# Performance work log

Measured on AMD Instinct MI355X. Metric: run time of the kernel, lower is better.

Reference implementation:

```python
import jax, jax.numpy as jnp
import numpy as np
from jax import lax

B, DIM, H, W = 8, 256, 48, 48
HEADS, DH = 8, 32
K, S = 5, 2
P = K // 2
SCALE = DH ** -0.5
EPS = 1e-5


def setup_inputs() -> dict:
    key = jax.random.key(0)
    ks = jax.random.split(key, 12)
    w = lambda k, sh: jax.random.normal(k, sh, jnp.float32) * 0.02
    return {
        'x': jax.random.normal(ks[0], (B, DIM, H, W), jnp.float32),
        'kv': jax.random.normal(ks[1], (B, DIM, H, W), jnp.float32),
        'wq': w(ks[2], (DIM, DIM)), 'bq': jnp.zeros((DIM,), jnp.float32),
        'wk': w(ks[3], (DIM, DIM)), 'bk': jnp.zeros((DIM,), jnp.float32),
        'wv': w(ks[4], (DIM, DIM)), 'bv': jnp.zeros((DIM,), jnp.float32),
        'w_dw': w(ks[5], (DH, 1, K, K)), 'b_dw': jnp.zeros((DH,), jnp.float32),
        'ln_w': jnp.ones((DH,), jnp.float32), 'ln_b': jnp.zeros((DH,), jnp.float32),
        'w_off': w(ks[6], (2, DH)),
        'wo': w(ks[7], (DIM, DIM)), 'bo': jnp.zeros((DIM,), jnp.float32),
    }


def conv1x1(x, w, b=None):
    # x: (B, Cin, H, W), w: (Cout, Cin)
    y = jnp.einsum('oc,bchw->bohw', w, x)
    return y if b is None else y + b[None, :, None, None]


def grid_sample_bilinear(inp, grid):
    # inp: (N, C, Hh, Ww); grid: (N, Hg, Wg, 2) in (x, y), align_corners=True
    N, C, Hh, Ww = inp.shape
    gx = (grid[..., 0] + 1.0) * 0.5 * (Ww - 1)
    gy = (grid[..., 1] + 1.0) * 0.5 * (Hh - 1)
    x0 = jnp.floor(gx)
    y0 = jnp.floor(gy)
    wx = gx - x0  # frac weights for x1/y1 corners
    wy = gy - y0
    x0i = jnp.clip(x0.astype(jnp.int32), 0, Ww - 1)
    x1i = jnp.clip(x0.astype(jnp.int32) + 1, 0, Ww - 1)
    y0i = jnp.clip(y0.astype(jnp.int32), 0, Hh - 1)
    y1i = jnp.clip(y0.astype(jnp.int32) + 1, 0, Hh - 1)
    flat = inp.reshape(N, C, Hh * Ww)
    n = grid.shape[1] * grid.shape[2]

    def gather(yi, xi):
        idx = (yi * Ww + xi).reshape(N, 1, n)
        return jnp.take_along_axis(flat, jnp.broadcast_to(idx, (N, C, n)), axis=2)

    w00 = ((1 - wx) * (1 - wy)).reshape(N, 1, n)
    w01 = (wx * (1 - wy)).reshape(N, 1, n)
    w10 = ((1 - wx) * wy).reshape(N, 1, n)
    w11 = (wx * wy).reshape(N, 1, n)
    return (w00 * gather(y0i, x0i) + w01 * gather(y0i, x1i)
            + w10 * gather(y1i, x0i) + w11 * gather(y1i, x1i))  # (N, C, n)


def reference(x, kv, wq, bq, wk, bk, wv, bv, w_dw, b_dw, ln_w, ln_b, w_off, wo, bo):
    q = conv1x1(x, wq, bq)                      # (B, DIM, H, W)
    q_off = q.reshape(B * HEADS, DH, H, W)      # per-head channels
    # depthwise offset conv
    t = lax.conv_general_dilated(q_off, w_dw, (S, S), [(P, P), (P, P)],
                                 feature_group_count=DH,
                                 dimension_numbers=('NCHW', 'OIHW', 'NCHW'))
    t = t + b_dw[None, :, None, None]
    Hk, Wk = t.shape[2], t.shape[3]
    n = Hk * Wk
    # LayerNormProxy: LN over channel dim
    t = t.transpose(0, 2, 3, 1)                 # (BH, Hk, Wk, DH)
    mu = t.mean(-1, keepdims=True)
    var = ((t - mu) ** 2).mean(-1, keepdims=True)
    t = (t - mu) / jnp.sqrt(var + EPS) * ln_w + ln_b
    t = jax.nn.gelu(t, approximate=False)
    offset = jnp.einsum('oc,bhwc->bhwo', w_off, t)  # (BH, Hk, Wk, 2) as (y, x)
    # reference points, normalized to [-1, 1]
    ref_y = (jnp.linspace(0.5, Hk - 0.5, Hk, dtype=jnp.float32) / (Hk - 1.0)) * 2.0 - 1.0
    ref_x = (jnp.linspace(0.5, Wk - 0.5, Wk, dtype=jnp.float32) / (Wk - 1.0)) * 2.0 - 1.0
    ref = jnp.stack(jnp.meshgrid(ref_y, ref_x, indexing='ij'), axis=-1)  # (Hk, Wk, 2)
    pos = jnp.clip(offset + ref[None], -1.0, 1.0)
    grid = pos[..., ::-1]                       # (x, y) order for sampling
    kvs = grid_sample_bilinear(kv.reshape(B * HEADS, DH, H, W), grid)  # (BH, DH, n)
    kv4 = kvs.reshape(B, DIM, 1, n)
    k = conv1x1(kv4, wk, bk).reshape(B * HEADS, DH, n)
    v = conv1x1(kv4, wv, bv).reshape(B * HEADS, DH, n)
    qf = q.reshape(B * HEADS, DH, H * W)
    attn = jax.nn.softmax(jnp.einsum('bcm,bcn->bmn', qf, k) * SCALE, axis=2)
    out = jnp.einsum('bmn,bcn->bcm', attn, v).reshape(B, DIM, H, W)
    return conv1x1(out, wo, bo)
```

## Files before the change

### kernel.cpp

```cpp
#include <hip/hip_runtime.h>
#include <hip/hip_bf16.h>
#include <cstddef>

#define BB 8
#define DIM 256
#define HH 48
#define WW 48
#define HW 2304
#define HEADS 8
#define DH 32
#define BH 64
#define HK 24
#define WK 24
#define NN 576
#define SCALE 0.17677669529663687f
#define EPSF 1e-5f

typedef __attribute__((ext_vector_type(8))) short short8;
typedef __attribute__((ext_vector_type(4))) float f32x4;

static __device__ inline short f2bf_s(float f) {
  __hip_bfloat16 h = __float2bfloat16(f);
  return *reinterpret_cast<short*>(&h);
}

static __device__ inline unsigned pkrnd(float a, float b) {
  unsigned ua = __builtin_bit_cast(unsigned, a) + 0x8000u;
  unsigned ub = __builtin_bit_cast(unsigned, b) + 0x8000u;
  return __builtin_amdgcn_perm(ub, ua, 0x07060302);
}

static __device__ inline void split8(const float* xf, short8& bh, short8& bl) {
  union { unsigned u[4]; short8 v; } H, L;
#pragma unroll
  for (int p = 0; p < 4; p++) {
    float x0 = xf[2 * p], x1 = xf[2 * p + 1];
    unsigned u0 = __builtin_bit_cast(unsigned, x0) & 0xffff0000u;
    unsigned u1 = __builtin_bit_cast(unsigned, x1) & 0xffff0000u;
    float l0 = x0 - __builtin_bit_cast(float, u0);
    float l1 = x1 - __builtin_bit_cast(float, u1);
    H.u[p] = __builtin_amdgcn_perm(u1, u0, 0x07060302);
    L.u[p] = __builtin_amdgcn_perm(__builtin_bit_cast(unsigned, l1),
                                   __builtin_bit_cast(unsigned, l0), 0x07060302);
  }
  bh = H.v;
  bl = L.v;
}

__global__ __launch_bounds__(512) void gemm_q_fused(
    const float* __restrict__ wq, const float* __restrict__ bias,
    const float* __restrict__ x, float* __restrict__ Y,
    const float* __restrict__ kv, float* __restrict__ kvT) {
  __shared__ float sLDS[16384];
  float* s_raw = sLDS;
  short* s_h   = (short*)(sLDS + 8192);
  short* s_l   = ((short*)(sLDS + 8192)) + 8192;
  const int bid = blockIdx.x;
  const int tid = threadIdx.x;

  if (bid < 288) {
    const int b = bid / 36;
    const int mBase = (bid % 36) * 64;
    const int wave = tid >> 6, lane = tid & 63;
    const int quad = lane >> 4, l15 = lane & 15;
    const int oBase = wave * 32;
    const int cm = tid & 63, cg = tid >> 6;
    const int ck0 = cg * 2, ck1 = cg * 2 + 1;
    const int cvt0 = cm * 128 + ((ck0 ^ (cm & 7)) << 3);
    const int cvt1 = cm * 128 + ((ck1 ^ (cm & 7)) << 3);

    f32x4 acc[2][4] = {};

    {
      const float* xb = x + ((size_t)b * 256) * HW + mBase;
#pragma unroll
      for (int it = 0; it < 4; it++) {
        int u = it * 512 + tid;
        int c = u >> 4, f4 = u & 15;
        *(float4*)(&s_raw[c * 64 + f4 * 4]) =
            *(const float4*)(xb + (size_t)c * HW + f4 * 4);
      }
    }
    __syncthreads();

    for (int half = 0; half < 2; half++) {
      {
        float vals[16];
#pragma unroll
        for (int i = 0; i < 16; i++) vals[i] = s_raw[(cg * 16 + i) * 64 + cm];
        short8 h0, l0, h1, l1;
        split8(vals, h0, l0);
        split8(vals + 8, h1, l1);
        *(short8*)(&s_h[cvt0]) = h0;
        *(short8*)(&s_l[cvt0]) = l0;
        *(short8*)(&s_h[cvt1]) = h1;
        *(short8*)(&s_l[cvt1]) = l1;
      }
      __syncthreads();

      if (half == 0) {
        const float* xb = x + ((size_t)b * 256 + 128) * HW + mBase;
#pragma unroll
        for (int it = 0; it < 4; it++) {
          int u = it * 512 + tid;
          int c = u >> 4, f4 = u & 15;
          *(float4*)(&s_raw[c * 64 + f4 * 4]) =
              *(const float4*)(xb + (size_t)c * HW + f4 * 4);
        }
      }

      for (int kc = 0; kc < 128; kc += 32) {
        short8 ah[2], al[2];
#pragma unroll
        for (int os = 0; os < 2; os++) {
          const float* wrow = wq + (size_t)(oBase + os * 16 + l15) * 256 +
                              half * 128 + kc + quad * 8;
          float w8[8];
          *(float4*)(w8) = *(const float4*)(wrow);
          *(float4*)(w8 + 4) = *(const float4*)(wrow + 4);
          split8(w8, ah[os], al[os]);
        }
#pragma unroll
        for (int mt = 0; mt < 4; mt++) {
          int row = mt * 16 + l15;
          int off = row * 128 + ((((kc >> 3) + quad) ^ (row & 7)) << 3);
          short8 bh_ = *(const short8*)(&s_h[off]);
          short8 bl_ = *(const short8*)(&s_l[off]);
#pragma unroll
          for (int os = 0; os < 2; os++) {
            acc[os][mt] = __builtin_amdgcn_mfma_f32_16x16x32_bf16(ah[os], bh_, acc[os][mt], 0, 0, 0);
            acc[os][mt] = __builtin_amdgcn_mfma_f32_16x16x32_bf16(al[os], bh_, acc[os][mt], 0, 0, 0);
            acc[os][mt] = __builtin_amdgcn_mfma_f32_16x16x32_bf16(ah[os], bl_, acc[os][mt], 0, 0, 0);
          }
        }
      }
      __syncthreads();
    }

#pragma unroll
    for (int os = 0; os < 2; os++)
#pragma unroll
      for (int r = 0; r < 4; r++) {
        int o = oBase + os * 16 + quad * 4 + r;
        float bs = bias[o];
        float* yp = Y + ((size_t)b * 256 + o) * HW + mBase + l15;
#pragma unroll
        for (int mt = 0; mt < 4; mt++) yp[mt * 16] = acc[os][mt][r] + bs;
      }
  } else {
    float* tf = sLDS;
    int bb = bid - 288;
    int mt = bb % 36, t2 = bb / 36;
    int ct = t2 & 3, b = t2 >> 2;
    const int c0 = ct * 64, m0 = mt * 64;
    const int col = tid & 63, row8 = tid >> 6;
    const float* xb = kv + ((size_t)b * 256 + c0) * HW + m0;
#pragma unroll
    for (int k = 0; k < 8; k++) {
      int c = row8 + k * 8;
      tf[c * 65 + col] = xb[(size_t)c * HW + col];
    }
    __syncthreads();
    float* ot = kvT + ((size_t)b * HW + m0) * 256 + c0;
#pragma unroll
    for (int k = 0; k < 8; k++) {
      int m = row8 + k * 8;
      ot[(size_t)m * 256 + col] = tf[col * 65 + m];
    }
  }
}

#define QPS 101
__global__ __launch_bounds__(256) void dw_sample_kernel(
    const float* __restrict__ q, const float* __restrict__ kvT,
    const float* __restrict__ w_dw, const float* __restrict__ b_dw,
    const float* __restrict__ ln_w, const float* __restrict__ ln_b,
    const float* __restrict__ w_off, short* __restrict__ kvsTh,
    short* __restrict__ kvsTl) {
  __shared__ float s_q[32 * QPS];
  __shared__ float s_w[DH * 25];
  const int tid = threadIdx.x;
  const int ch = tid & 31;
  const int np = tid >> 5;
  const int bid = blockIdx.x;
  const int b = bid & 7;
  const int r = bid >> 3;
  const int head = r / 72;
  const int rr = r - head * 72;
  const int yk = rr / 3;
  const int xk0 = (rr - yk * 3) * 8;
  const int bh = b * 8 + head;
  const int xk = xk0 + np;
  const int n = yk * WK + xk;

  for (int i = tid; i < DH * 25; i += 256) s_w[i] = w_dw[i];

  {
    const int y0 = yk * 2 - 2, x0 = xk0 * 2 - 2;
    const float* qbh = q + (size_t)bh * DH * HW;
#pragma unroll
    for (int it = 0; it < 13; it++) {
      int e = it * 256 + tid;
      if (e < 3200) {
        int c = e / 100;
        int rem = e - c * 100;
        int dy = rem / 20;
        int xl = rem - dy * 20;
        int gy = y0 + dy, gx = x0 + xl;
        float v = 0.f;
        if ((unsigned)gy < HH && (unsigned)gx < WW)
          v = qbh[(size_t)c * HW + gy * WW + gx];
        s_q[c * QPS + dy * 20 + xl] = v;
      }
    }
  }
  __syncthreads();

  float t = b_dw[ch];
  {
    const float* wp = s_w + ch * 25;
    const float* qp = s_q + ch * QPS + np * 2;
#pragma unroll
    for (int dy = 0; dy < 5; dy++)
#pragma unroll
      for (int dx = 0; dx < 5; dx++)
        t += wp[dy * 5 + dx] * qp[dy * 20 + dx];
  }

  float mu = t;
#pragma unroll
  for (int m = 1; m < 32; m <<= 1) mu += __shfl_xor(mu, m);
  mu *= (1.0f / DH);
  float d = t - mu;
  float var = d * d;
#pragma unroll
  for (int m = 1; m < 32; m <<= 1) var += __shfl_xor(var, m);
  var *= (1.0f / DH);
  float rstd = rsqrtf(var + EPSF);

  float xn = d * rstd * ln_w[ch] + ln_b[ch];
  float g = 0.5f * xn * (1.0f + erff(xn * 0.70710678118654752f));
  float o0 = w_off[ch] * g;
  float o1 = w_off[DH + ch] * g;
#pragma unroll
  for (int m = 1; m < 32; m <<= 1) {
    o0 += __shfl_xor(o0, m);
    o1 += __shfl_xor(o1, m);
  }

  const float ref_y = (0.5f + (float)yk) / 23.0f * 2.0f - 1.0f;
  const float ref_x = (0.5f + (float)xk) / 23.0f * 2.0f - 1.0f;
  float py = fminf(fmaxf(o0 + ref_y, -1.0f), 1.0f);
  float px = fminf(fmaxf(o1 + ref_x, -1.0f), 1.0f);

  float gx = (px + 1.0f) * 0.5f * 47.0f;
  float gy = (py + 1.0f) * 0.5f * 47.0f;
  float x0f = floorf(gx), y0f = floorf(gy);
  float wx = gx - x0f, wy = gy - y0f;
  int x0 = (int)x0f, y0 = (int)y0f;
  int x0i = min(max(x0, 0), WW - 1);
  int x1i = min(max(x0 + 1, 0), WW - 1);
  int y0i = min(max(y0, 0), HH - 1);
  int y1i = min(max(y0 + 1, 0), HH - 1);
  float w00 = (1.f - wx) * (1.f - wy);
  float w01 = wx * (1.f - wy);
  float w10 = (1.f - wx) * wy;
  float w11 = wx * wy;

  const float* kvb = kvT + (size_t)b * HW * 256 + head * DH + ch;
  float val = w00 * kvb[(size_t)(y0i * WW + x0i) * 256]
            + w01 * kvb[(size_t)(y0i * WW + x1i) * 256]
            + w10 * kvb[(size_t)(y1i * WW + x0i) * 256]
            + w11 * kvb[(size_t)(y1i * WW + x1i) * 256];

  unsigned ub = __builtin_bit_cast(unsigned, val);
  unsigned uh = ub & 0xffff0000u;
  float rem = val - __builtin_bit_cast(float, uh);
  size_t idx = ((size_t)b * NN + n) * 256 + head * DH + ch;
  kvsTh[idx] = (short)(uh >> 16);
  kvsTl[idx] = (short)(__builtin_bit_cast(unsigned, rem) >> 16);
}

__global__ __launch_bounds__(256) void kv_gemm_mfma(
    const float* __restrict__ wk, const float* __restrict__ bk,
    const float* __restrict__ wv, const float* __restrict__ bv,
    const short* __restrict__ Xh, const short* __restrict__ Xl,
    short* __restrict__ Kb, short* __restrict__ Vb) {
  const int tid = threadIdx.x;
  const int wave = tid >> 6;
  const int lane = tid & 63;
  const int quad = lane >> 4, l15 = lane & 15;
  const int b = blockIdx.z;
  const int mode = blockIdx.y >> 2;
  const int oTile = (blockIdx.y & 3) * 64;
  const int nBase = blockIdx.x * 64;

  if (mode == 0) {
    const int nW = nBase + wave * 16;
    const short* arh = Xh + ((size_t)b * NN + nW + l15) * 256 + quad * 8;
    const short* arl = Xl + ((size_t)b * NN + nW + l15) * 256 + quad * 8;
    f32x4 acc[4] = {};
    for (int kc = 0; kc < 256; kc += 32) {
      short8 ah = *(const short8*)(arh + kc);
      short8 al = *(const short8*)(arl + kc);
#pragma unroll
      for (int ot = 0; ot < 4; ot++) {
        const float* wrow = wk + (size_t)(oTile + ot * 16 + l15) * 256 + kc + quad * 8;
        float w8[8];
        *(float4*)(w8) = *(const float4*)(wrow);
        *(float4*)(w8 + 4) = *(const float4*)(wrow + 4);
        short8 bh_, bl_;
        split8(w8, bh_, bl_);
        acc[ot] = __builtin_amdgcn_mfma_f32_16x16x32_bf16(ah, bh_, acc[ot], 0, 0, 0);
        acc[ot] = __builtin_amdgcn_mfma_f32_16x16x32_bf16(al, bh_, acc[ot], 0, 0, 0);
        acc[ot] = __builtin_amdgcn_mfma_f32_16x16x32_bf16(ah, bl_, acc[ot], 0, 0, 0);
      }
    }
    float bs[4];
#pragma unroll
    for (int ot = 0; ot < 4; ot++) bs[ot] = bk[oTile + ot * 16 + l15];
#pragma unroll
    for (int r = 0; r < 4; r++) {
      short* yp = Kb + ((size_t)b * NN + nW + quad * 4 + r) * 256 + oTile + l15;
#pragma unroll
      for (int ot = 0; ot < 4; ot++) yp[ot * 16] = f2bf_s(acc[ot][r] + bs[ot]);
    }
  } else {
    const int oW = oTile + wave * 16;
    const float* wrow = wv + (size_t)(oW + l15) * 256 + quad * 8;
    f32x4 acc[4] = {};
    for (int kc = 0; kc < 256; kc += 32) {
      float w8[8];
      *(float4*)(w8) = *(const float4*)(wrow + kc);
      *(float4*)(w8 + 4) = *(const float4*)(wrow + kc + 4);
      short8 ah, al;
      split8(w8, ah, al);
#pragma unroll
      for (int nt = 0; nt < 4; nt++) {
        short8 bh_ = *(const short8*)(Xh + ((size_t)b * NN + nBase + nt * 16 + l15) * 256 + kc + quad * 8);
        short8 bl_ = *(const short8*)(Xl + ((size_t)b * NN + nBase + nt * 16 + l15) * 256 + kc + quad * 8);
        acc[nt] = __builtin_amdgcn_mfma_f32_16x16x32_bf16(ah, bh_, acc[nt], 0, 0, 0);
        acc[nt] = __builtin_amdgcn_mfma_f32_16x16x32_bf16(al, bh_, acc[nt], 0, 0, 0);
        acc[nt] = __builtin_amdgcn_mfma_f32_16x16x32_bf16(ah, bl_, acc[nt], 0, 0, 0);
      }
    }
#pragma unroll
    for (int r = 0; r < 4; r++) {
      int o = oW + quad * 4 + r;
      float bs = bv[o];
      short* yp = Vb + ((size_t)b * 256 + o) * NN + nBase + l15;
#pragma unroll
      for (int nt = 0; nt < 4; nt++) yp[nt * 16] = f2bf_s(acc[nt][r] + bs);
    }
  }
}

__global__ __launch_bounds__(256) void attn_mfma(const float* __restrict__ q,
                                                 const short* __restrict__ Kb,
                                                 const short* __restrict__ Vb,
                                                 short* __restrict__ O) {
  __shared__ short sK[2][64 * 40];
  __shared__ short sV[2][32 * 88];
  __shared__ int sP[4][2][256];
  const int tid = threadIdx.x;
  const int wave = tid >> 6;
  const int lane = tid & 63;
  const int quad = lane >> 4;
  const int l15 = lane & 15;
  const int bh = blockIdx.y;
  const int b = bh >> 3, head = bh & 7;
  const int mBase = blockIdx.x * 128 + wave * 32;

  short8 bq[2];
#pragma unroll
  for (int mt = 0; mt < 2; mt++) {
    const float* qp = q + ((size_t)bh * DH + quad * 8) * HW + mBase + mt * 16 + l15;
    short8 v;
#pragma unroll
    for (int j = 0; j < 8; j++) v[j] = f2bf_s(qp[(size_t)j * HW] * SCALE);
    bq[mt] = v;
  }

  const int kn = tid >> 2, kc = (tid & 3) * 8;
  const int vc = tid >> 3, vn = (tid & 7) * 8;
  const short* kg = Kb + (size_t)b * NN * 256 + head * DH;
  const short* vg = Vb + ((size_t)b * 256 + head * DH) * NN;

  short8 kreg = *(const short8*)(kg + (size_t)kn * 256 + kc);
  short8 vreg = *(const short8*)(vg + (size_t)vc * NN + vn);
  *(short8*)(&sK[0][kn * 40 + kc]) = kreg;
  *(short8*)(&sV[0][vc * 88 + vn]) = vreg;
  __syncthreads();

  const int g = (l15 >> 1) & 3;
  const int row16 = l15 * 16;
  const int wr0 = row16 + (((quad >> 1) ^ g) << 2) + ((quad & 1) << 1);
  const int wr1 = row16 + (((2 + (quad >> 1)) ^ g) << 2) + ((quad & 1) << 1);
  const int rd = row16 + ((quad ^ g) << 2);

  f32x4 oacc[2][2] = {};
  f32x4 dacc[2] = {};
  const short ONE = 0x3F80;
  const short8 ones = {ONE, ONE, ONE, ONE, ONE, ONE, ONE, ONE};

  for (int s = 0; s < 9; s++) {
    const int buf = s & 1;
    if (s + 1 < 9) {
      kreg = *(const short8*)(kg + (size_t)((s + 1) * 64 + kn) * 256 + kc);
      vreg = *(const short8*)(vg + (size_t)vc * NN + (s + 1) * 64 + vn);
    }
#pragma unroll
    for (int nt = 0; nt < 2; nt++) {
      short8 ka0 = *(const short8*)(&sK[buf][(nt * 32 + l15) * 40 + quad * 8]);
      short8 ka1 = *(const short8*)(&sK[buf][(nt * 32 + 16 + l15) * 40 + quad * 8]);
      short8 va0 = *(const short8*)(&sV[buf][l15 * 88 + nt * 32 + quad * 8]);
      short8 va1 = *(const short8*)(&sV[buf][(16 + l15) * 88 + nt * 32 + quad * 8]);
      f32x4 z = {0.f, 0.f, 0.f, 0.f};
      f32x4 st[2][2];
      st[0][0] = __builtin_amdgcn_mfma_f32_16x16x32_bf16(ka0, bq[0], z, 0, 0, 0);
      st[0][1] = __builtin_amdgcn_mfma_f32_16x16x32_bf16(ka1, bq[0], z, 0, 0, 0);
      st[1][0] = __builtin_amdgcn_mfma_f32_16x16x32_bf16(ka0, bq[1], z, 0, 0, 0);
      st[1][1] = __builtin_amdgcn_mfma_f32_16x16x32_bf16(ka1, bq[1], z, 0, 0, 0);
#pragma unroll
      for (int mt = 0; mt < 2; mt++) {
        float p0 = __expf(st[mt][0][0]), p1 = __expf(st[mt][0][1]);
        float p2 = __expf(st[mt][0][2]), p3 = __expf(st[mt][0][3]);
        float p4 = __expf(st[mt][1][0]), p5 = __expf(st[mt][1][1]);
        float p6 = __expf(st[mt][1][2]), p7 = __expf(st[mt][1][3]);
        int* base = &sP[wave][mt][0];
        *(int2*)(base + wr0) = make_int2((int)pkrnd(p0, p1), (int)pkrnd(p2, p3));
        *(int2*)(base + wr1) = make_int2((int)pkrnd(p4, p5), (int)pkrnd(p6, p7));
      }
#pragma unroll
      for (int mt = 0; mt < 2; mt++) {
        short8 pa = *(short8*)(&sP[wave][mt][0] + rd);
        oacc[mt][0] = __builtin_amdgcn_mfma_f32_16x16x32_bf16(pa, va0, oacc[mt][0], 0, 0, 0);
        oacc[mt][1] = __builtin_amdgcn_mfma_f32_16x16x32_bf16(pa, va1, oacc[mt][1], 0, 0, 0);
        dacc[mt] = __builtin_amdgcn_mfma_f32_16x16x32_bf16(pa, ones, dacc[mt], 0, 0, 0);
      }
    }
    if (s + 1 < 9) {
      *(short8*)(&sK[buf ^ 1][kn * 40 + kc]) = kreg;
      *(short8*)(&sV[buf ^ 1][vc * 88 + vn]) = vreg;
    }
    __syncthreads();
  }

#pragma unroll
  for (int mt = 0; mt < 2; mt++) {
    short* ob = O + ((size_t)b * HW + mBase + mt * 16) * 256 + head * DH + l15;
#pragma unroll
    for (int r = 0; r < 4; r++) {
      float inv = 1.0f / dacc[mt][r];
      ob[(size_t)(quad * 4 + r) * 256] = f2bf_s(oacc[mt][0][r] * inv);
      ob[(size_t)(quad * 4 + r) * 256 + 16] = f2bf_s(oacc[mt][1][r] * inv);
    }
  }
}

__global__ __launch_bounds__(512) void wo_gemm_mfma(const float* __restrict__ wo,
                                                    const float* __restrict__ bias,
                                                    const short* __restrict__ X,
                                                    float* __restrict__ Y) {
  __shared__ short sX[64 * 256];
  const int tid = threadIdx.x;
  const int b = blockIdx.y;
  const int mBase = blockIdx.x * 64;

  const short* src = X + ((size_t)b * HW + mBase) * 256;
#pragma unroll
  for (int it = 0; it < 4; it++) {
    int idx = it * 512 + tid;
    int row = idx >> 5, ck = idx & 31;
    *(short8*)(&sX[row * 256 + ((ck ^ (row & 7)) << 3)]) =
        *(const short8*)(src + (size_t)row * 256 + ck * 8);
  }
  __syncthreads();

  const int wave = tid >> 6, lane = tid & 63;
  const int quad = lane >> 4, l15 = lane & 15;
  const int oBase = wave * 32;

  f32x4 acc[2][4] = {};
  for (int kc = 0; kc < 256; kc += 32) {
    short8 ah[2], al[2];
#pragma unroll
    for (int os = 0; os < 2; os++) {
      const float* wrow = wo + (size_t)(oBase + os * 16 + l15) * 256 + kc + quad * 8;
      float w8[8];
      *(float4*)(w8) = *(const float4*)(wrow);
      *(float4*)(w8 + 4) = *(const float4*)(wrow + 4);
      split8(w8, ah[os], al[os]);
    }
#pragma unroll
    for (int mt = 0; mt < 4; mt++) {
      int row = mt * 16 + l15;
      short8 bx = *(const short8*)(&sX[row * 256 + ((((kc >> 3) + quad) ^ (row & 7)) << 3)]);
#pragma unroll
      for (int os = 0; os < 2; os++) {
        acc[os][mt] = __builtin_amdgcn_mfma_f32_16x16x32_bf16(ah[os], bx, acc[os][mt], 0, 0, 0);
        acc[os][mt] = __builtin_amdgcn_mfma_f32_16x16x32_bf16(al[os], bx, acc[os][mt], 0, 0, 0);
      }
    }
  }

#pragma unroll
  for (int os = 0; os < 2; os++)
#pragma unroll
    for (int r = 0; r < 4; r++) {
      int o = oBase + os * 16 + quad * 4 + r;
      float bs = bias[o];
      float* yp = Y + ((size_t)b * 256 + o) * HW + mBase + l15;
#pragma unroll
      for (int mt = 0; mt < 4; mt++) yp[mt * 16] = acc[os][mt][r] + bs;
    }
}

extern "C" void kernel_launch(void* const* d_in, const int* in_sizes, int n_in,
                              void* d_out, int out_size, void* d_ws, size_t ws_size,
                              hipStream_t stream) {
  const float* x    = (const float*)d_in[0];
  const float* kv   = (const float*)d_in[1];
  const float* wq   = (const float*)d_in[2];
  const float* bq   = (const float*)d_in[3];
  const float* wk   = (const float*)d_in[4];
  const float* bk   = (const float*)d_in[5];
  const float* wv   = (const float*)d_in[6];
  const float* bv   = (const float*)d_in[7];
  const float* w_dw = (const float*)d_in[8];
  const float* b_dw = (const float*)d_in[9];
  const float* ln_w = (const float*)d_in[10];
  const float* ln_b = (const float*)d_in[11];
  const float* w_off= (const float*)d_in[12];
  const float* wo   = (const float*)d_in[13];
  const float* bo   = (const float*)d_in[14];
  float* out = (float*)d_out;
  float* ws = (float*)d_ws;

  float* q     = ws;
  short* O     = (short*)(ws + 4718592);
  short* kvsTh = (short*)(ws + 7077888);
  short* kvsTl = (short*)(ws + 7667712);
  short* Kb    = (short*)(ws + 8257536);
  short* Vb    = (short*)(ws + 8847360);
  float* kvT = out;

  gemm_q_fused<<<dim3(1440), dim3(512), 0, stream>>>(wq, bq, x, q, kv, kvT);
  dw_sample_kernel<<<dim3(BH * NN / 8), dim3(256), 0, stream>>>(
      q, kvT, w_dw, b_dw, ln_w, ln_b, w_off, kvsTh, kvsTl);
  kv_gemm_mfma<<<dim3(NN / 64, 8, BB), dim3(256), 0, stream>>>(
      wk, bk, wv, bv, kvsTh, kvsTl, Kb, Vb);
  attn_mfma<<<dim3(HW / 128, BH), dim3(256), 0, stream>>>(q, Kb, Vb, O);
  wo_gemm_mfma<<<dim3(HW / 64, BB), dim3(512), 0, stream>>>(wo, bo, O, out);
}
```

Measured before the change: 222.0 us.

## Shrink LDS in Q GEMM and split output GEMM into smaller tiles

```diff
diff --git a/kernel.cpp b/kernel.cpp
--- a/kernel.cpp
+++ b/kernel.cpp
@@ -51,10 +51,9 @@
     const float* __restrict__ wq, const float* __restrict__ bias,
     const float* __restrict__ x, float* __restrict__ Y,
     const float* __restrict__ kv, float* __restrict__ kvT) {
-  __shared__ float sLDS[16384];
-  float* s_raw = sLDS;
-  short* s_h   = (short*)(sLDS + 8192);
-  short* s_l   = ((short*)(sLDS + 8192)) + 8192;
+  __shared__ float s_raw[64 * 65];
+  __shared__ short s_h[64 * 64];
+  __shared__ short s_l[64 * 64];
   const int bid = blockIdx.x;
   const int tid = threadIdx.x;
 
@@ -64,57 +63,53 @@
     const int wave = tid >> 6, lane = tid & 63;
     const int quad = lane >> 4, l15 = lane & 15;
     const int oBase = wave * 32;
-    const int cm = tid & 63, cg = tid >> 6;
-    const int ck0 = cg * 2, ck1 = cg * 2 + 1;
-    const int cvt0 = cm * 128 + ((ck0 ^ (cm & 7)) << 3);
-    const int cvt1 = cm * 128 + ((ck1 ^ (cm & 7)) << 3);
+    const int cm = tid >> 3, cck = tid & 7;
+    const int cvt = cm * 64 + ((cck ^ (cm & 7)) << 3);
 
     f32x4 acc[2][4] = {};
 
     {
       const float* xb = x + ((size_t)b * 256) * HW + mBase;
 #pragma unroll
-      for (int it = 0; it < 4; it++) {
+      for (int it = 0; it < 2; it++) {
         int u = it * 512 + tid;
         int c = u >> 4, f4 = u & 15;
-        *(float4*)(&s_raw[c * 64 + f4 * 4]) =
+        *(float4*)(&s_raw[c * 65 + f4 * 4]) =
             *(const float4*)(xb + (size_t)c * HW + f4 * 4);
       }
     }
     __syncthreads();
 
-    for (int half = 0; half < 2; half++) {
+    for (int qtr = 0; qtr < 4; qtr++) {
       {
-        float vals[16];
-#pragma unroll
-        for (int i = 0; i < 16; i++) vals[i] = s_raw[(cg * 16 + i) * 64 + cm];
-        short8 h0, l0, h1, l1;
+        float vals[8];
+#pragma unroll
+        for (int j = 0; j < 8; j++) vals[j] = s_raw[(cck * 8 + j) * 65 + cm];
+        short8 h0, l0;
         split8(vals, h0, l0);
-        split8(vals + 8, h1, l1);
-        *(short8*)(&s_h[cvt0]) = h0;
-        *(short8*)(&s_l[cvt0]) = l0;
-        *(short8*)(&s_h[cvt1]) = h1;
-        *(short8*)(&s_l[cvt1]) = l1;
+        *(short8*)(&s_h[cvt]) = h0;
+        *(short8*)(&s_l[cvt]) = l0;
       }
       __syncthreads();
 
-      if (half == 0) {
-        const float* xb = x + ((size_t)b * 256 + 128) * HW + mBase;
-#pragma unroll
-        for (int it = 0; it < 4; it++) {
+      if (qtr < 3) {
+        const float* xb = x + ((size_t)b * 256 + (qtr + 1) * 64) * HW + mBase;
+#pragma unroll
+        for (int it = 0; it < 2; it++) {
           int u = it * 512 + tid;
           int c = u >> 4, f4 = u & 15;
-          *(float4*)(&s_raw[c * 64 + f4 * 4]) =
+          *(float4*)(&s_raw[c * 65 + f4 * 4]) =
               *(const float4*)(xb + (size_t)c * HW + f4 * 4);
         }
       }
 
-      for (int kc = 0; kc < 128; kc += 32) {
+#pragma unroll
+      for (int kk = 0; kk < 2; kk++) {
+        const int kc = qtr * 64 + kk * 32;
         short8 ah[2], al[2];
 #pragma unroll
         for (int os = 0; os < 2; os++) {
-          const float* wrow = wq + (size_t)(oBase + os * 16 + l15) * 256 +
-                              half * 128 + kc + quad * 8;
+          const float* wrow = wq + (size_t)(oBase + os * 16 + l15) * 256 + kc + quad * 8;
           float w8[8];
           *(float4*)(w8) = *(const float4*)(wrow);
           *(float4*)(w8 + 4) = *(const float4*)(wrow + 4);
@@ -123,7 +118,7 @@
 #pragma unroll
         for (int mt = 0; mt < 4; mt++) {
           int row = mt * 16 + l15;
-          int off = row * 128 + ((((kc >> 3) + quad) ^ (row & 7)) << 3);
+          int off = row * 64 + ((((kk << 2) + quad) ^ (row & 7)) << 3);
           short8 bh_ = *(const short8*)(&s_h[off]);
           short8 bl_ = *(const short8*)(&s_l[off]);
 #pragma unroll
@@ -148,7 +143,6 @@
         for (int mt = 0; mt < 4; mt++) yp[mt * 16] = acc[os][mt][r] + bs;
       }
   } else {
-    float* tf = sLDS;
     int bb = bid - 288;
     int mt = bb % 36, t2 = bb / 36;
     int ct = t2 & 3, b = t2 >> 2;
@@ -158,14 +152,14 @@
 #pragma unroll
     for (int k = 0; k < 8; k++) {
       int c = row8 + k * 8;
-      tf[c * 65 + col] = xb[(size_t)c * HW + col];
+      s_raw[c * 65 + col] = xb[(size_t)c * HW + col];
     }
     __syncthreads();
     float* ot = kvT + ((size_t)b * HW + m0) * 256 + c0;
 #pragma unroll
     for (int k = 0; k < 8; k++) {
       int m = row8 + k * 8;
-      ot[(size_t)m * 256 + col] = tf[col * 65 + m];
+      ot[(size_t)m * 256 + col] = s_raw[col * 65 + m];
     }
   }
 }
@@ -458,19 +452,20 @@
   }
 }
 
-__global__ __launch_bounds__(512) void wo_gemm_mfma(const float* __restrict__ wo,
+__global__ __launch_bounds__(256) void wo_gemm_mfma(const float* __restrict__ wo,
                                                     const float* __restrict__ bias,
                                                     const short* __restrict__ X,
                                                     float* __restrict__ Y) {
-  __shared__ short sX[64 * 256];
+  __shared__ short sX[32 * 256];
   const int tid = threadIdx.x;
-  const int b = blockIdx.y;
-  const int mBase = blockIdx.x * 64;
+  const int b = blockIdx.z;
+  const int oHalf = blockIdx.y * 128;
+  const int mBase = blockIdx.x * 32;
 
   const short* src = X + ((size_t)b * HW + mBase) * 256;
 #pragma unroll
   for (int it = 0; it < 4; it++) {
-    int idx = it * 512 + tid;
+    int idx = it * 256 + tid;
     int row = idx >> 5, ck = idx & 31;
     *(short8*)(&sX[row * 256 + ((ck ^ (row & 7)) << 3)]) =
         *(const short8*)(src + (size_t)row * 256 + ck * 8);
@@ -479,9 +474,9 @@
 
   const int wave = tid >> 6, lane = tid & 63;
   const int quad = lane >> 4, l15 = lane & 15;
-  const int oBase = wave * 32;
-
-  f32x4 acc[2][4] = {};
+  const int oBase = oHalf + wave * 32;
+
+  f32x4 acc[2][2] = {};
   for (int kc = 0; kc < 256; kc += 32) {
     short8 ah[2], al[2];
 #pragma unroll
@@ -493,7 +488,7 @@
       split8(w8, ah[os], al[os]);
     }
 #pragma unroll
-    for (int mt = 0; mt < 4; mt++) {
+    for (int mt = 0; mt < 2; mt++) {
       int row = mt * 16 + l15;
       short8 bx = *(const short8*)(&sX[row * 256 + ((((kc >> 3) + quad) ^ (row & 7)) << 3)]);
 #pragma unroll
@@ -512,7 +507,7 @@
       float bs = bias[o];
       float* yp = Y + ((size_t)b * 256 + o) * HW + mBase + l15;
 #pragma unroll
-      for (int mt = 0; mt < 4; mt++) yp[mt * 16] = acc[os][mt][r] + bs;
+      for (int mt = 0; mt < 2; mt++) yp[mt * 16] = acc[os][mt][r] + bs;
     }
 }
 
@@ -551,5 +546,5 @@
   kv_gemm_mfma<<<dim3(NN / 64, 8, BB), dim3(256), 0, stream>>>(
       wk, bk, wv, bv, kvsTh, kvsTl, Kb, Vb);
   attn_mfma<<<dim3(HW / 128, BH), dim3(256), 0, stream>>>(q, Kb, Vb, O);
-  wo_gemm_mfma<<<dim3(HW / 64, BB), dim3(512), 0, stream>>>(wo, bo, O, out);
-}
+  wo_gemm_mfma<<<dim3(72, 2, BB), dim3(256), 0, stream>>>(wo, bo, O, out);
+}
```

Result: no change. 226.3 us (+2.0%).
